# Kernel optimization log

Measured on AMD Instinct MI355X. Metric: run time of the kernel, lower is better.

Reference implementation:

```python
import jax, jax.numpy as jnp
import numpy as np

NUM_ENVS = 16384
N = 12          # decision vars (4 legs x 3D force)
M_CON = 24      # 4 SOC cones (3 each) + 12-dim hardtanh box
A_MIN, A_MAX = -10.0, 10.0
ALPHA, BETA = 1.0, 1.0


def setup_inputs() -> dict:
    key = jax.random.key(0)
    k1, k2, k3, k4 = jax.random.split(key, 4)
    Mw = jax.random.normal(k1, (NUM_ENVS, N, N), dtype=jnp.float32) / np.sqrt(N)
    # P must be SPD for inv/solve as in the original QP setup
    P = Mw @ jnp.swapaxes(Mw, -1, -2) + jnp.eye(N, dtype=jnp.float32)
    q = jax.random.normal(k2, (NUM_ENVS, N), dtype=jnp.float32)
    H = jax.random.normal(k3, (NUM_ENVS, M_CON, N), dtype=jnp.float32) * 0.5
    b = jax.random.normal(k4, (NUM_ENVS, M_CON), dtype=jnp.float32)
    contact_filter = jnp.ones((NUM_ENVS, M_CON), dtype=jnp.float32)
    return {"P": P, "q": q, "H": H, "b": b, "contact_filter": contact_filter, "iters": 100}


def _project(z, cf):
    # z: [B, m, 1]. Faithful to torch: project_onto_soc's only in-place effect on z
    # is z_part *= (z_part[:, 2:3] > 0); the full cone projection result is
    # discarded (returned but never written back). Then hardtanh box, then contact filter.
    Bsz = z.shape[0]
    soc = z[:, :12].reshape(Bsz, 4, 3)               # 4 cones of dim 3
    soc = soc * (soc[:, :, 2:3] > 0)                 # zero cone block if z-component <= 0
    box = jnp.clip(z[:, 12:24], A_MIN, A_MAX)        # hardtanh
    z = jnp.concatenate([soc.reshape(Bsz, 12, 1), box], axis=1)
    return z * cf


def reference(P, q, H, b, contact_filter, iters):
    m = H.shape[1]
    q_ = q[..., None]                                # [B, n, 1]
    b_ = b[..., None]                                # [B, m, 1]
    cf = contact_filter[..., None]                   # [B, m, 1]
    Ht = jnp.swapaxes(H, -1, -2)
    I = jnp.eye(m, dtype=P.dtype)
    Fm = I - H @ jnp.linalg.inv(P + Ht @ H) @ Ht     # [B, m, m]
    mu = Fm @ (H @ jnp.linalg.solve(P, q_) - b_)     # [B, m, 1]
    A = jnp.concatenate([
        jnp.concatenate([Fm, BETA * Fm], axis=2),
        jnp.concatenate([ALPHA * (I - 2.0 * Fm), I - 2.0 * ALPHA * BETA * Fm], axis=2),
    ], axis=1)                                       # [B, 2m, 2m]
    Bv = jnp.concatenate([BETA * mu, -2.0 * ALPHA * BETA * mu], axis=1)  # [B, 2m, 1]

    def step(lz, _):
        lz = A @ lz + Bv
        lz = jnp.concatenate([lz[:, :m], _project(lz[:, m:], cf)], axis=1)
        return lz, None

    lz0 = jnp.zeros((P.shape[0], 2 * m, 1), dtype=P.dtype)
    lz, _ = jax.lax.scan(step, lz0, None, length=iters)
    x = jnp.linalg.pinv(H) @ (lz[:, m:] - b_)        # [B, n, 1]
    return x, lz
```

## Files before the change

kernel.cpp:

```cpp
#include <hip/hip_runtime.h>

#define EPB 32
#define BLOCK 256
#define HS 292
#define GS 148
#define SS 28

#define WFENCE() __builtin_amdgcn_wave_barrier()

#define DPP_XOR1 0xB1
#define DPP_XOR2 0x4E
#define DPP_HMIR 0x141

constexpr int GMAP[8] = {0, 1, 2, 3, 7, 6, 5, 4};

typedef float f2 __attribute__((ext_vector_type(2)));

__device__ __forceinline__ f2 pkfma(f2 a, f2 b, f2 c) {
  return __builtin_elementwise_fma(a, b, c);
}

#define FMA4(acc, f, s)                                         \
  acc = fmaf((f).x, (s).x,                                      \
        fmaf((f).y, (s).y,                                      \
        fmaf((f).z, (s).z,                                      \
        fmaf((f).w, (s).w, (acc)))))

#define VFMA(acc, s, v)                                         \
  { (acc).x = fmaf((s), (v).x, (acc).x);                        \
    (acc).y = fmaf((s), (v).y, (acc).y);                        \
    (acc).z = fmaf((s), (v).z, (acc).z);                        \
    (acc).w = fmaf((s), (v).w, (acc).w); }

#define ADD4(A, B) { (A).x += (B).x; (A).y += (B).y; (A).z += (B).z; (A).w += (B).w; }

template<int CTRL>
__device__ __forceinline__ float dppv(float v) {
  return __int_as_float(__builtin_amdgcn_update_dpp(
      0, __float_as_int(v), CTRL, 0xF, 0xF, true));
}

template<int K>
__device__ __forceinline__ float getel(const float4& a, const float4& b, const float4& c) {
  if constexpr (K == 0) return a.x; else if constexpr (K == 1) return a.y;
  else if constexpr (K == 2) return a.z; else if constexpr (K == 3) return a.w;
  else if constexpr (K == 4) return b.x; else if constexpr (K == 5) return b.y;
  else if constexpr (K == 6) return b.z; else if constexpr (K == 7) return b.w;
  else if constexpr (K == 8) return c.x; else if constexpr (K == 9) return c.y;
  else if constexpr (K == 10) return c.z; else return c.w;
}
template<int K>
__device__ __forceinline__ void setel(float4& a, float4& b, float4& c, float v) {
  if constexpr (K == 0) a.x = v; else if constexpr (K == 1) a.y = v;
  else if constexpr (K == 2) a.z = v; else if constexpr (K == 3) a.w = v;
  else if constexpr (K == 4) b.x = v; else if constexpr (K == 5) b.y = v;
  else if constexpr (K == 6) b.z = v; else if constexpr (K == 7) b.w = v;
  else if constexpr (K == 8) c.x = v; else if constexpr (K == 9) c.y = v;
  else if constexpr (K == 10) c.z = v; else c.w = v;
}

template<int S>
__device__ __forceinline__ void putS2(f2* m, float v) {
  if constexpr ((S & 1) == 0) m[S / 2].x = v; else m[S / 2].y = v;
}

#define PMQ(pm, Q) make_float4(pm[2*(Q)].x, pm[2*(Q)].y, pm[2*(Q)+1].x, pm[2*(Q)+1].y)

__device__ __forceinline__ float dot12(float4 a0, float4 a1, float4 a2,
                                       const float* p) {
  const float4* p4 = (const float4*)p;
  float4 b0 = p4[0], b1 = p4[1], b2 = p4[2];
  float acc = 0.f;
  FMA4(acc, a0, b0); FMA4(acc, a1, b1); FMA4(acc, a2, b2);
  return acc;
}

template<int K>
__device__ __forceinline__ void pivot_pub(float4& a, float4& b, float4& c, float* piv) {
  float ip = 1.0f / getel<K>(a, b, c);
  setel<K>(a, b, c, 1.0f);
  a.x *= ip; a.y *= ip; a.z *= ip; a.w *= ip;
  b.x *= ip; b.y *= ip; b.z *= ip; b.w *= ip;
  c.x *= ip; c.y *= ip; c.z *= ip; c.w *= ip;
  float4* pv = (float4*)piv;
  pv[0] = a; pv[1] = b; pv[2] = c;
}

#define ELIM(f, A, B, C)                                              \
  { (A).x = fmaf(-(f), p0.x, (A).x); (A).y = fmaf(-(f), p0.y, (A).y); \
    (A).z = fmaf(-(f), p0.z, (A).z); (A).w = fmaf(-(f), p0.w, (A).w); \
    (B).x = fmaf(-(f), p1.x, (B).x); (B).y = fmaf(-(f), p1.y, (B).y); \
    (B).z = fmaf(-(f), p1.z, (B).z); (B).w = fmaf(-(f), p1.w, (B).w); \
    (C).x = fmaf(-(f), p2.x, (C).x); (C).y = fmaf(-(f), p2.y, (C).y); \
    (C).z = fmaf(-(f), p2.z, (C).z); (C).w = fmaf(-(f), p2.w, (C).w); }

template<int K>
__device__ __forceinline__ void rgj_step(float4& a0, float4& b0, float4& c0,
                                         float4& a1, float4& b1, float4& c1,
                                         float* piv, int t) {
  if constexpr (K < 8) {
    if (t == K) pivot_pub<K>(a0, b0, c0, piv);
  } else {
    if (t == K - 8) pivot_pub<K>(a1, b1, c1, piv);
  }
  WFENCE();
  const float4* pv = (const float4*)piv;
  float4 p0 = pv[0], p1 = pv[1], p2 = pv[2];
  {
    const bool own = (K < 8) && (t == K);
    float cur = getel<K>(a0, b0, c0);
    float f = own ? 0.0f : cur;
    setel<K>(a0, b0, c0, own ? cur : 0.0f);
    ELIM(f, a0, b0, c0);
  }
  {
    const bool own = (K >= 8) && (t == K - 8);
    float cur = getel<K>(a1, b1, c1);
    float f = own ? 0.0f : cur;
    setel<K>(a1, b1, c1, own ? cur : 0.0f);
    ELIM(f, a1, b1, c1);
  }
  WFENCE();
}

template<int K>
__device__ __forceinline__ void rgj_all(float4& a0, float4& b0, float4& c0,
                                        float4& a1, float4& b1, float4& c1,
                                        float* piv, int t) {
  rgj_step<K>(a0, b0, c0, a1, b1, c1, piv, t);
  if constexpr (K < 11) rgj_all<K + 1>(a0, b0, c0, a1, b1, c1, piv, t);
}

__device__ __forceinline__ void gram_rows(const float* myH, int t, int i1,
    float4& a0, float4& b0, float4& c0, float4& a1, float4& b1, float4& c1) {
  a0 = make_float4(0.f, 0.f, 0.f, 0.f);
  b0 = a0; c0 = a0; a1 = a0; b1 = a0; c1 = a0;
#pragma unroll
  for (int k = 0; k < 24; ++k) {
    const float4* hk = (const float4*)(myH + k * 12);
    float4 h0 = hk[0], h1 = hk[1], h2 = hk[2];
    float f0 = myH[k * 12 + t];
    float f1 = myH[k * 12 + i1];
    VFMA(a0, f0, h0); VFMA(b0, f0, h1); VFMA(c0, f0, h2);
    VFMA(a1, f1, h0); VFMA(b1, f1, h1); VFMA(c1, f1, h2);
  }
}

template<int g, int k>
__device__ __forceinline__ void slot3(const float* myH, int t,
    const float4* W0, const float4* W1, const float4* W2,
    f2* P0, f2* P1, f2* P2) {
  const int c = 3 * (t ^ GMAP[g]) + k;
  const float4* hc = (const float4*)(myH + c * 12);
  float4 h0 = hc[0], h1 = hc[1], h2 = hc[2];
  float d0 = 0.f, d1 = 0.f, d2 = 0.f;
  FMA4(d0, h0, W0[0]); FMA4(d0, h1, W0[1]); FMA4(d0, h2, W0[2]);
  FMA4(d1, h0, W1[0]); FMA4(d1, h1, W1[1]); FMA4(d1, h2, W1[2]);
  FMA4(d2, h0, W2[0]); FMA4(d2, h1, W2[1]); FMA4(d2, h2, W2[2]);
  constexpr int S = 3 * g + k;
  putS2<S>(P0, ((g == 0 && k == 0) ? 1.0f : 0.0f) - d0);
  putS2<S>(P1, ((g == 0 && k == 1) ? 1.0f : 0.0f) - d1);
  putS2<S>(P2, ((g == 0 && k == 2) ? 1.0f : 0.0f) - d2);
}

template<int S>
__device__ __forceinline__ float bgat(const float* bB, int t) {
  constexpr int g = S / 3, k = S % 3;
  return bB[3 * (t ^ GMAP[g]) + k];
}

__global__ __attribute__((amdgpu_flat_work_group_size(BLOCK, BLOCK),
                          amdgpu_waves_per_eu(1, 4)))
void pdhg_kernel(const float* __restrict__ P, const float* __restrict__ q,
                 const float* __restrict__ H, const float* __restrict__ b,
                 const float* __restrict__ cf, const int* __restrict__ itp,
                 float* __restrict__ out, int Btot) {
  __shared__ __align__(16) float sH[EPB * HS];
  __shared__ __align__(16) float sGi[EPB * GS];
  __shared__ __align__(16) float sB[EPB * SS];
  __shared__ __align__(16) float sAux[EPB * SS];

  const int tid  = threadIdx.x;
  const int wq   = tid >> 6;
  const int lane = tid & 63;
  const int e    = wq * 8 + (lane >> 3);
  const int t    = lane & 7;
  const int env  = blockIdx.x * EPB + e;
  const int envW0 = blockIdx.x * EPB + wq * 8;
  const int niter = itp[0];
  const int r0w = 3 * t;
  const int i1 = (t < 4) ? t + 8 : t;

  {
    const float4* gH = (const float4*)(H + (size_t)envW0 * 288);
#pragma unroll
    for (int rep = 0; rep < 9; ++rep) {
      int i = lane + rep * 64;
      int ee = i / 72, off = i - ee * 72;
      *(float4*)&sH[(wq * 8 + ee) * HS + off * 4] = gH[i];
    }
    const float4* gP = (const float4*)(P + (size_t)envW0 * 144);
#pragma unroll
    for (int rep = 0; rep < 4; ++rep) {
      int i = lane + rep * 64;
      int ee = i / 36, off = i - ee * 36;
      *(float4*)&sGi[(wq * 8 + ee) * GS + off * 4] = gP[i];
    }
    { int i = lane + 256; if (lane < 32) {
        int ee = i / 36, off = i - ee * 36;
        *(float4*)&sGi[(wq * 8 + ee) * GS + off * 4] = gP[i]; } }
    const float4* gq = (const float4*)(q + (size_t)envW0 * 12);
    if (lane < 24) {
      int ee = lane / 3, off = lane - ee * 3;
      *(float4*)&sAux[(wq * 8 + ee) * SS + off * 4] = gq[lane];
    }
    const float4* gb = (const float4*)(b + (size_t)envW0 * 24);
    if (lane < 48) {
      int ee = lane / 6, off = lane - ee * 6;
      *(float4*)&sB[(wq * 8 + ee) * SS + off * 4] = gb[lane];
    }
  }
  WFENCE();

  const float* myH = &sH[e * HS];
  float* giB  = &sGi[e * GS];
  float* auxB = &sAux[e * SS];
  float* bBm  = &sB[e * SS];
  const float* bB = bBm;

  float4 g0a, g0b, g0c, g1a, g1b, g1c;
  gram_rows(myH, t, i1, g0a, g0b, g0c, g1a, g1b, g1c);
  {
    const float4* p0 = (const float4*)(giB + t * 12);
    const float4* p1 = (const float4*)(giB + i1 * 12);
    float4 q0 = p0[0], q1 = p0[1], q2 = p0[2];
    float4 r0 = p1[0], r1 = p1[1], r2 = p1[2];
    ADD4(g0a, q0); ADD4(g0b, q1); ADD4(g0c, q2);
    ADD4(g1a, r0); ADD4(g1b, r1); ADD4(g1c, r2);
  }
  rgj_all<0>(g0a, g0b, g0c, g1a, g1b, g1c, auxB + 12, t);

  {
    float4* w0 = (float4*)(giB + t * 12);
    w0[0] = g0a; w0[1] = g0b; w0[2] = g0c;
    if (t < 4) {
      float4* w1 = (float4*)(giB + (t + 8) * 12);
      w1[0] = g1a; w1[1] = g1b; w1[2] = g1c;
    }
  }
  float y0 = dot12(g0a, g0b, g0c, auxB);
  float y1 = dot12(g1a, g1b, g1c, auxB);
  WFENCE();
  auxB[12 + t] = y0;
  if (t < 4) auxB[20 + t] = y1;
  WFENCE();

  float4 hr0[3], hr1[3], hr2[3];
  { const float4* p = (const float4*)(myH + (r0w + 0) * 12); hr0[0]=p[0]; hr0[1]=p[1]; hr0[2]=p[2]; }
  { const float4* p = (const float4*)(myH + (r0w + 1) * 12); hr1[0]=p[0]; hr1[1]=p[1]; hr1[2]=p[2]; }
  { const float4* p = (const float4*)(myH + (r0w + 2) * 12); hr2[0]=p[0]; hr2[1]=p[1]; hr2[2]=p[2]; }
  float u0, u1, u2;
  {
    const float4* y4 = (const float4*)(auxB + 12);
    float4 ya = y4[0], yb = y4[1], yc = y4[2];
    u0 = 0.f; FMA4(u0, hr0[0], ya); FMA4(u0, hr0[1], yb); FMA4(u0, hr0[2], yc);
    u1 = 0.f; FMA4(u1, hr1[0], ya); FMA4(u1, hr1[1], yb); FMA4(u1, hr1[2], yc);
    u2 = 0.f; FMA4(u2, hr2[0], ya); FMA4(u2, hr2[1], yb); FMA4(u2, hr2[2], yc);
  }

  float4 W0[3], W1[3], W2[3];
  W0[0] = make_float4(0.f,0.f,0.f,0.f); W0[1] = W0[0]; W0[2] = W0[0];
  W1[0] = W0[0]; W1[1] = W0[0]; W1[2] = W0[0];
  W2[0] = W0[0]; W2[1] = W0[0]; W2[2] = W0[0];
#define ACC_W(c, EX)                                                   \
  { const float4* g4 = (const float4*)(giB + (c) * 12);                \
    float4 r0 = g4[0], r1 = g4[1], r2 = g4[2];                         \
    float k0 = hr0[(c) >> 2].EX, k1 = hr1[(c) >> 2].EX, k2 = hr2[(c) >> 2].EX; \
    VFMA(W0[0], k0, r0); VFMA(W0[1], k0, r1); VFMA(W0[2], k0, r2);     \
    VFMA(W1[0], k1, r0); VFMA(W1[1], k1, r1); VFMA(W1[2], k1, r2);     \
    VFMA(W2[0], k2, r0); VFMA(W2[1], k2, r1); VFMA(W2[2], k2, r2); }
  ACC_W(0, x) ACC_W(1, y) ACC_W(2,  z) ACC_W(3,  w)
  ACC_W(4, x) ACC_W(5, y) ACC_W(6,  z) ACC_W(7,  w)
  ACC_W(8, x) ACC_W(9, y) ACC_W(10, z) ACC_W(11, w)
#undef ACC_W

  f2 pm0[12], pm1[12], pm2[12];
#define SL(g, k) slot3<g, k>(myH, t, W0, W1, W2, pm0, pm1, pm2);
  SL(0,0) SL(0,1) SL(0,2)  SL(1,0) SL(1,1) SL(1,2)
  SL(2,0) SL(2,1) SL(2,2)  SL(3,0) SL(3,1) SL(3,2)
  SL(4,0) SL(4,1) SL(4,2)  SL(5,0) SL(5,1) SL(5,2)
  SL(6,0) SL(6,1) SL(6,2)  SL(7,0) SL(7,1) SL(7,2)
#undef SL

  float mu0, mu1, mu2;
  {
    float4 bg0 = make_float4(bgat<0>(bB,t),  bgat<1>(bB,t),  bgat<2>(bB,t),  bgat<3>(bB,t));
    float4 bg1 = make_float4(bgat<4>(bB,t),  bgat<5>(bB,t),  bgat<6>(bB,t),  bgat<7>(bB,t));
    float4 bg2 = make_float4(bgat<8>(bB,t),  bgat<9>(bB,t),  bgat<10>(bB,t), bgat<11>(bB,t));
    float4 bg3 = make_float4(bgat<12>(bB,t), bgat<13>(bB,t), bgat<14>(bB,t), bgat<15>(bB,t));
    float4 bg4 = make_float4(bgat<16>(bB,t), bgat<17>(bB,t), bgat<18>(bB,t), bgat<19>(bB,t));
    float4 bg5 = make_float4(bgat<20>(bB,t), bgat<21>(bB,t), bgat<22>(bB,t), bgat<23>(bB,t));
    float d0 = 0.f, d1 = 0.f, d2 = 0.f;
    FMA4(d0, PMQ(pm0,0), bg0); FMA4(d1, PMQ(pm1,0), bg0); FMA4(d2, PMQ(pm2,0), bg0);
    FMA4(d0, PMQ(pm0,1), bg1); FMA4(d1, PMQ(pm1,1), bg1); FMA4(d2, PMQ(pm2,1), bg1);
    FMA4(d0, PMQ(pm0,2), bg2); FMA4(d1, PMQ(pm1,2), bg2); FMA4(d2, PMQ(pm2,2), bg2);
    FMA4(d0, PMQ(pm0,3), bg3); FMA4(d1, PMQ(pm1,3), bg3); FMA4(d2, PMQ(pm2,3), bg3);
    FMA4(d0, PMQ(pm0,4), bg4); FMA4(d1, PMQ(pm1,4), bg4); FMA4(d2, PMQ(pm2,4), bg4);
    FMA4(d0, PMQ(pm0,5), bg5); FMA4(d1, PMQ(pm1,5), bg5); FMA4(d2, PMQ(pm2,5), bg5);
    mu0 = u0 - d0;
    mu1 = u1 - d1;
    mu2 = u2 - d2;
  }
  float cfr0 = cf[(size_t)env * 24 + r0w];
  float cfr1 = cf[(size_t)env * 24 + r0w + 1];
  float cfr2 = cf[(size_t)env * 24 + r0w + 2];

  const float plo  = (t < 4) ? -3.0e38f : -10.0f;
  const float phi  = (t < 4) ?  3.0e38f :  10.0f;
  const float pthr = (t < 4) ? 0.0f     : -3.0e38f;
  float l0 = 0.f, l1 = 0.f, l2 = 0.f, z0 = 0.f, z1 = 0.f, z2 = 0.f;
#pragma unroll 2
  for (int it = 0; it < niter; ++it) {
    float s0 = l0 + z0, s1 = l1 + z1, s2 = l2 + z2;
    float g3  = dppv<DPP_XOR1>(s0), g4  = dppv<DPP_XOR1>(s1), g5  = dppv<DPP_XOR1>(s2);
    float g6  = dppv<DPP_XOR2>(s0), g7  = dppv<DPP_XOR2>(s1), g8  = dppv<DPP_XOR2>(s2);
    float g12 = dppv<DPP_HMIR>(s0), g13 = dppv<DPP_HMIR>(s1), g14 = dppv<DPP_HMIR>(s2);
    f2 vp0 = {s0, s1};
    f2 A0 = {mu0, 0.f}, A1 = {mu1, 0.f}, A2 = {mu2, 0.f};
    A0 = pkfma(pm0[0], vp0, A0); A1 = pkfma(pm1[0], vp0, A1); A2 = pkfma(pm2[0], vp0, A2);
    float g9  = dppv<DPP_XOR2>(g3),  g10 = dppv<DPP_XOR2>(g4),  g11 = dppv<DPP_XOR2>(g5);
    float g15 = dppv<DPP_HMIR>(g3),  g16 = dppv<DPP_HMIR>(g4),  g17 = dppv<DPP_HMIR>(g5);
    float g18 = dppv<DPP_HMIR>(g6),  g19 = dppv<DPP_HMIR>(g7),  g20 = dppv<DPP_HMIR>(g8);
    f2 vp1 = {s2, g3}, vp2 = {g4, g5}, vp3 = {g6, g7};
    A0 = pkfma(pm0[1], vp1, A0); A1 = pkfma(pm1[1], vp1, A1); A2 = pkfma(pm2[1], vp1, A2);
    A0 = pkfma(pm0[2], vp2, A0); A1 = pkfma(pm1[2], vp2, A1); A2 = pkfma(pm2[2], vp2, A2);
    A0 = pkfma(pm0[3], vp3, A0); A1 = pkfma(pm1[3], vp3, A1); A2 = pkfma(pm2[3], vp3, A2);
    float g21 = dppv<DPP_HMIR>(g9), g22 = dppv<DPP_HMIR>(g10), g23 = dppv<DPP_HMIR>(g11);
    f2 vp4 = {g8, g9}, vp5 = {g10, g11};
    A0 = pkfma(pm0[4], vp4, A0); A1 = pkfma(pm1[4], vp4, A1); A2 = pkfma(pm2[4], vp4, A2);
    A0 = pkfma(pm0[5], vp5, A0); A1 = pkfma(pm1[5], vp5, A1); A2 = pkfma(pm2[5], vp5, A2);
    f2 vp6 = {g12, g13}, vp7 = {g14, g15}, vp8 = {g16, g17}, vp9 = {g18, g19};
    f2 B0 = {0.f, 0.f}, B1 = {0.f, 0.f}, B2 = {0.f, 0.f};
    B0 = pkfma(pm0[6], vp6, B0); B1 = pkfma(pm1[6], vp6, B1); B2 = pkfma(pm2[6], vp6, B2);
    B0 = pkfma(pm0[7], vp7, B0); B1 = pkfma(pm1[7], vp7, B1); B2 = pkfma(pm2[7], vp7, B2);
    B0 = pkfma(pm0[8], vp8, B0); B1 = pkfma(pm1[8], vp8, B1); B2 = pkfma(pm2[8], vp8, B2);
    B0 = pkfma(pm0[9], vp9, B0); B1 = pkfma(pm1[9], vp9, B1); B2 = pkfma(pm2[9], vp9, B2);
    f2 vp10 = {g20, g21}, vp11 = {g22, g23};
    B0 = pkfma(pm0[10], vp10, B0); B1 = pkfma(pm1[10], vp10, B1); B2 = pkfma(pm2[10], vp10, B2);
    B0 = pkfma(pm0[11], vp11, B0); B1 = pkfma(pm1[11], vp11, B1); B2 = pkfma(pm2[11], vp11, B2);
    f2 C0 = A0 + B0, C1 = A1 + B1, C2 = A2 + B2;
    float w0 = C0.x + C0.y, w1 = C1.x + C1.y, w2 = C2.x + C2.y;
    float zp0 = fmaf(-2.0f, w0, s0);
    float zp1 = fmaf(-2.0f, w1, s1);
    float zp2 = fmaf(-2.0f, w2, s2);
    l0 = w0; l1 = w1; l2 = w2;
    bool gt = zp2 > pthr;
    float e0 = gt ? cfr0 : 0.0f;
    float e1 = gt ? cfr1 : 0.0f;
    float e2 = gt ? cfr2 : 0.0f;
    z0 = __builtin_amdgcn_fmed3f(zp0, plo, phi) * e0;
    z1 = __builtin_amdgcn_fmed3f(zp1, plo, phi) * e1;
    z2 = __builtin_amdgcn_fmed3f(zp2, plo, phi) * e2;
  }

  float* xout  = out;
  float* lzout = out + (size_t)Btot * 12;
  lzout[(size_t)env * 48 + r0w]          = l0;
  lzout[(size_t)env * 48 + r0w + 1]      = l1;
  lzout[(size_t)env * 48 + r0w + 2]      = l2;
  lzout[(size_t)env * 48 + 24 + r0w]     = z0;
  lzout[(size_t)env * 48 + 24 + r0w + 1] = z1;
  lzout[(size_t)env * 48 + 24 + r0w + 2] = z2;

  float bo0 = bB[r0w];
  float bo1 = bB[r0w + 1];
  float bo2 = bB[r0w + 2];
  WFENCE();
  auxB[r0w]     = z0 - bo0;
  auxB[r0w + 1] = z1 - bo1;
  auxB[r0w + 2] = z2 - bo2;
  WFENCE();

  float rv0 = 0.f, rv8 = 0.f;
  {
    const float4* a4 = (const float4*)auxB;
    float4 au0 = a4[0], au1 = a4[1], au2 = a4[2], au3 = a4[3], au4 = a4[4], au5 = a4[5];
#define RVS(k, AV) { rv0 = fmaf(myH[(k) * 12 + t],  (AV), rv0);   \
                     rv8 = fmaf(myH[(k) * 12 + i1], (AV), rv8); }
    RVS(0,  au0.x) RVS(1,  au0.y) RVS(2,  au0.z) RVS(3,  au0.w)
    RVS(4,  au1.x) RVS(5,  au1.y) RVS(6,  au1.z) RVS(7,  au1.w)
    RVS(8,  au2.x) RVS(9,  au2.y) RVS(10, au2.z) RVS(11, au2.w)
    RVS(12, au3.x) RVS(13, au3.y) RVS(14, au3.z) RVS(15, au3.w)
    RVS(16, au4.x) RVS(17, au4.y) RVS(18, au4.z) RVS(19, au4.w)
    RVS(20, au5.x) RVS(21, au5.y) RVS(22, au5.z) RVS(23, au5.w)
#undef RVS
  }

  gram_rows(myH, t, i1, g0a, g0b, g0c, g1a, g1b, g1c);
  WFENCE();
  auxB[t] = rv0;
  if (t < 4) auxB[t + 8] = rv8;
  WFENCE();
  rgj_all<0>(g0a, g0b, g0c, g1a, g1b, g1c, bBm, t);

  xout[(size_t)env * 12 + t] = dot12(g0a, g0b, g0c, auxB);
  if (t < 4)
    xout[(size_t)env * 12 + t + 8] = dot12(g1a, g1b, g1c, auxB);
}

extern "C" void kernel_launch(void* const* d_in, const int* in_sizes, int n_in,
                              void* d_out, int out_size, void* d_ws, size_t ws_size,
                              hipStream_t stream) {
  const float* P  = (const float*)d_in[0];
  const float* q  = (const float*)d_in[1];
  const float* H  = (const float*)d_in[2];
  const float* b  = (const float*)d_in[3];
  const float* cf = (const float*)d_in[4];
  const int*   it = (const int*)d_in[5];
  float* out = (float*)d_out;
  const int B = in_sizes[1] / 12;
  const int grid = B / EPB;
  pdhg_kernel<<<grid, BLOCK, 0, stream>>>(P, q, H, b, cf, it, out, B);
}
```

Before: 139.6 us.

## Remap to four lanes per env with six rows each, halving block size

Each environment is now handled by 4 lanes instead of 8. Each lane owns 6 rows of the 24-row iteration matrix, using 72 packed coefficients instead of 36. The 128-thread block still covers 32 envs, so each wave processes 16 envs. The change drops the 8-lane DPP mirror gather in favour of quad-level XOR and quad-permute shuffles, and the Gauss-Jordan solve now spreads 3 rows per lane. This cuts cross-lane shuffles per useful FMA and removes the lane imbalance in the 12-row solves, at the cost of doubling register pressure for the coefficient arrays, which could lower occupancy or cause spills.

```diff
diff --git a/kernel.cpp b/kernel.cpp
--- a/kernel.cpp
+++ b/kernel.cpp
@@ -1,7 +1,7 @@
 #include <hip/hip_runtime.h>
 
 #define EPB 32
-#define BLOCK 256
+#define BLOCK 128
 #define HS 292
 #define GS 148
 #define SS 28
@@ -10,9 +10,7 @@
 
 #define DPP_XOR1 0xB1
 #define DPP_XOR2 0x4E
-#define DPP_HMIR 0x141
-
-constexpr int GMAP[8] = {0, 1, 2, 3, 7, 6, 5, 4};
+#define DPP_QP3  0x1B
 
 typedef float f2 __attribute__((ext_vector_type(2)));
 
@@ -58,13 +56,6 @@
   else if constexpr (K == 8) c.x = v; else if constexpr (K == 9) c.y = v;
   else if constexpr (K == 10) c.z = v; else c.w = v;
 }
-
-template<int S>
-__device__ __forceinline__ void putS2(f2* m, float v) {
-  if constexpr ((S & 1) == 0) m[S / 2].x = v; else m[S / 2].y = v;
-}
-
-#define PMQ(pm, Q) make_float4(pm[2*(Q)].x, pm[2*(Q)].y, pm[2*(Q)+1].x, pm[2*(Q)+1].y)
 
 __device__ __forceinline__ float dot12(float4 a0, float4 a1, float4 a2,
                                        const float* p) {
@@ -95,79 +86,135 @@
     (C).z = fmaf(-(f), p2.z, (C).z); (C).w = fmaf(-(f), p2.w, (C).w); }
 
 template<int K>
-__device__ __forceinline__ void rgj_step(float4& a0, float4& b0, float4& c0,
-                                         float4& a1, float4& b1, float4& c1,
-                                         float* piv, int t) {
-  if constexpr (K < 8) {
-    if (t == K) pivot_pub<K>(a0, b0, c0, piv);
-  } else {
-    if (t == K - 8) pivot_pub<K>(a1, b1, c1, piv);
+__device__ __forceinline__ void rgj3_step(
+    float4& a0, float4& b0, float4& c0,
+    float4& a1, float4& b1, float4& c1,
+    float4& a2, float4& b2, float4& c2,
+    float* piv, int t) {
+  constexpr int SET = K >> 2, OWN = K & 3;
+  if (t == OWN) {
+    if constexpr (SET == 0)      pivot_pub<K>(a0, b0, c0, piv);
+    else if constexpr (SET == 1) pivot_pub<K>(a1, b1, c1, piv);
+    else                         pivot_pub<K>(a2, b2, c2, piv);
   }
   WFENCE();
   const float4* pv = (const float4*)piv;
   float4 p0 = pv[0], p1 = pv[1], p2 = pv[2];
   {
-    const bool own = (K < 8) && (t == K);
+    const bool own = (SET == 0) && (t == OWN);
     float cur = getel<K>(a0, b0, c0);
     float f = own ? 0.0f : cur;
     setel<K>(a0, b0, c0, own ? cur : 0.0f);
     ELIM(f, a0, b0, c0);
   }
   {
-    const bool own = (K >= 8) && (t == K - 8);
+    const bool own = (SET == 1) && (t == OWN);
     float cur = getel<K>(a1, b1, c1);
     float f = own ? 0.0f : cur;
     setel<K>(a1, b1, c1, own ? cur : 0.0f);
     ELIM(f, a1, b1, c1);
   }
+  {
+    const bool own = (SET == 2) && (t == OWN);
+    float cur = getel<K>(a2, b2, c2);
+    float f = own ? 0.0f : cur;
+    setel<K>(a2, b2, c2, own ? cur : 0.0f);
+    ELIM(f, a2, b2, c2);
+  }
   WFENCE();
 }
 
 template<int K>
-__device__ __forceinline__ void rgj_all(float4& a0, float4& b0, float4& c0,
-                                        float4& a1, float4& b1, float4& c1,
-                                        float* piv, int t) {
-  rgj_step<K>(a0, b0, c0, a1, b1, c1, piv, t);
-  if constexpr (K < 11) rgj_all<K + 1>(a0, b0, c0, a1, b1, c1, piv, t);
-}
-
-__device__ __forceinline__ void gram_rows(const float* myH, int t, int i1,
-    float4& a0, float4& b0, float4& c0, float4& a1, float4& b1, float4& c1) {
+__device__ __forceinline__ void rgj3_all(
+    float4& a0, float4& b0, float4& c0,
+    float4& a1, float4& b1, float4& c1,
+    float4& a2, float4& b2, float4& c2,
+    float* piv, int t) {
+  rgj3_step<K>(a0, b0, c0, a1, b1, c1, a2, b2, c2, piv, t);
+  if constexpr (K < 11) rgj3_all<K + 1>(a0, b0, c0, a1, b1, c1, a2, b2, c2, piv, t);
+}
+
+__device__ __forceinline__ void gram3(const float* myH, int t,
+    float4& a0, float4& b0, float4& c0,
+    float4& a1, float4& b1, float4& c1,
+    float4& a2, float4& b2, float4& c2) {
   a0 = make_float4(0.f, 0.f, 0.f, 0.f);
-  b0 = a0; c0 = a0; a1 = a0; b1 = a0; c1 = a0;
+  b0 = a0; c0 = a0; a1 = a0; b1 = a0; c1 = a0; a2 = a0; b2 = a0; c2 = a0;
 #pragma unroll
   for (int k = 0; k < 24; ++k) {
     const float4* hk = (const float4*)(myH + k * 12);
     float4 h0 = hk[0], h1 = hk[1], h2 = hk[2];
     float f0 = myH[k * 12 + t];
-    float f1 = myH[k * 12 + i1];
-    VFMA(a0, f0, h0); VFMA(b0, f0, h1); VFMA(c0, f0, h2);
-    VFMA(a1, f1, h0); VFMA(b1, f1, h1); VFMA(c1, f1, h2);
-  }
-}
-
-template<int g, int k>
-__device__ __forceinline__ void slot3(const float* myH, int t,
-    const float4* W0, const float4* W1, const float4* W2,
-    f2* P0, f2* P1, f2* P2) {
-  const int c = 3 * (t ^ GMAP[g]) + k;
+    float f1 = myH[k * 12 + t + 4];
+    float f2v = myH[k * 12 + t + 8];
+    VFMA(a0, f0, h0);  VFMA(b0, f0, h1);  VFMA(c0, f0, h2);
+    VFMA(a1, f1, h0);  VFMA(b1, f1, h1);  VFMA(c1, f1, h2);
+    VFMA(a2, f2v, h0); VFMA(b2, f2v, h1); VFMA(c2, f2v, h2);
+  }
+}
+
+__device__ __forceinline__ void buildW(const float* myH, const float* gi, int r0,
+                                       float4* Wa, float4* Wb, float4* Wc) {
+  Wa[0] = make_float4(0.f, 0.f, 0.f, 0.f); Wa[1] = Wa[0]; Wa[2] = Wa[0];
+  Wb[0] = Wa[0]; Wb[1] = Wa[0]; Wb[2] = Wa[0];
+  Wc[0] = Wa[0]; Wc[1] = Wa[0]; Wc[2] = Wa[0];
+#pragma unroll
+  for (int c = 0; c < 12; ++c) {
+    const float4* g4 = (const float4*)(gi + c * 12);
+    float4 r0v = g4[0], r1v = g4[1], r2v = g4[2];
+    float k0 = myH[(r0 + 0) * 12 + c];
+    float k1 = myH[(r0 + 1) * 12 + c];
+    float k2 = myH[(r0 + 2) * 12 + c];
+    VFMA(Wa[0], k0, r0v); VFMA(Wa[1], k0, r1v); VFMA(Wa[2], k0, r2v);
+    VFMA(Wb[0], k1, r0v); VFMA(Wb[1], k1, r1v); VFMA(Wb[2], k1, r2v);
+    VFMA(Wc[0], k2, r0v); VFMA(Wc[1], k2, r1v); VFMA(Wc[2], k2, r2v);
+  }
+}
+
+template<int m, int k, int base>
+__device__ __forceinline__ void slot4(const float* myH, int t,
+    const float4* Wa, const float4* Wb, const float4* Wc,
+    f2* pA, f2* pB, f2* pC) {
+  const int c = 6 * (t ^ m) + k;
   const float4* hc = (const float4*)(myH + c * 12);
   float4 h0 = hc[0], h1 = hc[1], h2 = hc[2];
   float d0 = 0.f, d1 = 0.f, d2 = 0.f;
-  FMA4(d0, h0, W0[0]); FMA4(d0, h1, W0[1]); FMA4(d0, h2, W0[2]);
-  FMA4(d1, h0, W1[0]); FMA4(d1, h1, W1[1]); FMA4(d1, h2, W1[2]);
-  FMA4(d2, h0, W2[0]); FMA4(d2, h1, W2[1]); FMA4(d2, h2, W2[2]);
-  constexpr int S = 3 * g + k;
-  putS2<S>(P0, ((g == 0 && k == 0) ? 1.0f : 0.0f) - d0);
-  putS2<S>(P1, ((g == 0 && k == 1) ? 1.0f : 0.0f) - d1);
-  putS2<S>(P2, ((g == 0 && k == 2) ? 1.0f : 0.0f) - d2);
-}
-
-template<int S>
-__device__ __forceinline__ float bgat(const float* bB, int t) {
-  constexpr int g = S / 3, k = S % 3;
-  return bB[3 * (t ^ GMAP[g]) + k];
-}
+  FMA4(d0, h0, Wa[0]); FMA4(d0, h1, Wa[1]); FMA4(d0, h2, Wa[2]);
+  FMA4(d1, h0, Wb[0]); FMA4(d1, h1, Wb[1]); FMA4(d1, h2, Wb[2]);
+  FMA4(d2, h0, Wc[0]); FMA4(d2, h1, Wc[1]); FMA4(d2, h2, Wc[2]);
+  float v0 = ((m == 0 && k == base + 0) ? 1.0f : 0.0f) - d0;
+  float v1 = ((m == 0 && k == base + 1) ? 1.0f : 0.0f) - d1;
+  float v2 = ((m == 0 && k == base + 2) ? 1.0f : 0.0f) - d2;
+  constexpr int P = 3 * m + (k >> 1);
+  if constexpr ((k & 1) == 0) { pA[P].x = v0; pB[P].x = v1; pC[P].x = v2; }
+  else                        { pA[P].y = v0; pB[P].y = v1; pC[P].y = v2; }
+}
+
+#define SLOTS(base, pA, pB, pC)                                   \
+  slot4<0,0,base>(myH,t,Wa,Wb,Wc,pA,pB,pC);                       \
+  slot4<0,1,base>(myH,t,Wa,Wb,Wc,pA,pB,pC);                       \
+  slot4<0,2,base>(myH,t,Wa,Wb,Wc,pA,pB,pC);                       \
+  slot4<0,3,base>(myH,t,Wa,Wb,Wc,pA,pB,pC);                       \
+  slot4<0,4,base>(myH,t,Wa,Wb,Wc,pA,pB,pC);                       \
+  slot4<0,5,base>(myH,t,Wa,Wb,Wc,pA,pB,pC);                       \
+  slot4<1,0,base>(myH,t,Wa,Wb,Wc,pA,pB,pC);                       \
+  slot4<1,1,base>(myH,t,Wa,Wb,Wc,pA,pB,pC);                       \
+  slot4<1,2,base>(myH,t,Wa,Wb,Wc,pA,pB,pC);                       \
+  slot4<1,3,base>(myH,t,Wa,Wb,Wc,pA,pB,pC);                       \
+  slot4<1,4,base>(myH,t,Wa,Wb,Wc,pA,pB,pC);                       \
+  slot4<1,5,base>(myH,t,Wa,Wb,Wc,pA,pB,pC);                       \
+  slot4<2,0,base>(myH,t,Wa,Wb,Wc,pA,pB,pC);                       \
+  slot4<2,1,base>(myH,t,Wa,Wb,Wc,pA,pB,pC);                       \
+  slot4<2,2,base>(myH,t,Wa,Wb,Wc,pA,pB,pC);                       \
+  slot4<2,3,base>(myH,t,Wa,Wb,Wc,pA,pB,pC);                       \
+  slot4<2,4,base>(myH,t,Wa,Wb,Wc,pA,pB,pC);                       \
+  slot4<2,5,base>(myH,t,Wa,Wb,Wc,pA,pB,pC);                       \
+  slot4<3,0,base>(myH,t,Wa,Wb,Wc,pA,pB,pC);                       \
+  slot4<3,1,base>(myH,t,Wa,Wb,Wc,pA,pB,pC);                       \
+  slot4<3,2,base>(myH,t,Wa,Wb,Wc,pA,pB,pC);                       \
+  slot4<3,3,base>(myH,t,Wa,Wb,Wc,pA,pB,pC);                       \
+  slot4<3,4,base>(myH,t,Wa,Wb,Wc,pA,pB,pC);                       \
+  slot4<3,5,base>(myH,t,Wa,Wb,Wc,pA,pB,pC);
 
 __global__ __attribute__((amdgpu_flat_work_group_size(BLOCK, BLOCK),
                           amdgpu_waves_per_eu(1, 4)))
@@ -183,41 +230,44 @@
   const int tid  = threadIdx.x;
   const int wq   = tid >> 6;
   const int lane = tid & 63;
-  const int e    = wq * 8 + (lane >> 3);
-  const int t    = lane & 7;
+  const int g16  = lane >> 2;
+  const int t    = lane & 3;
+  const int e    = wq * 16 + g16;
   const int env  = blockIdx.x * EPB + e;
-  const int envW0 = blockIdx.x * EPB + wq * 8;
+  const int envW0 = blockIdx.x * EPB + wq * 16;
   const int niter = itp[0];
-  const int r0w = 3 * t;
-  const int i1 = (t < 4) ? t + 8 : t;
+  const int r6 = 6 * t;
 
   {
     const float4* gH = (const float4*)(H + (size_t)envW0 * 288);
+#pragma unroll
+    for (int rep = 0; rep < 18; ++rep) {
+      int i = lane + rep * 64;
+      int ee = i / 72, off = i - ee * 72;
+      *(float4*)&sH[(wq * 16 + ee) * HS + off * 4] = gH[i];
+    }
+    const float4* gP = (const float4*)(P + (size_t)envW0 * 144);
 #pragma unroll
     for (int rep = 0; rep < 9; ++rep) {
       int i = lane + rep * 64;
-      int ee = i / 72, off = i - ee * 72;
-      *(float4*)&sH[(wq * 8 + ee) * HS + off * 4] = gH[i];
+      int ee = i / 36, off = i - ee * 36;
+      *(float4*)&sGi[(wq * 16 + ee) * GS + off * 4] = gP[i];
     }
-    const float4* gP = (const float4*)(P + (size_t)envW0 * 144);
-#pragma unroll
-    for (int rep = 0; rep < 4; ++rep) {
-      int i = lane + rep * 64;
-      int ee = i / 36, off = i - ee * 36;
-      *(float4*)&sGi[(wq * 8 + ee) * GS + off * 4] = gP[i];
-    }
-    { int i = lane + 256; if (lane < 32) {
-        int ee = i / 36, off = i - ee * 36;
-        *(float4*)&sGi[(wq * 8 + ee) * GS + off * 4] = gP[i]; } }
     const float4* gq = (const float4*)(q + (size_t)envW0 * 12);
-    if (lane < 24) {
+    if (lane < 48) {
       int ee = lane / 3, off = lane - ee * 3;
-      *(float4*)&sAux[(wq * 8 + ee) * SS + off * 4] = gq[lane];
+      *(float4*)&sAux[(wq * 16 + ee) * SS + off * 4] = gq[lane];
     }
     const float4* gb = (const float4*)(b + (size_t)envW0 * 24);
-    if (lane < 48) {
-      int ee = lane / 6, off = lane - ee * 6;
-      *(float4*)&sB[(wq * 8 + ee) * SS + off * 4] = gb[lane];
+    {
+      int i = lane;
+      int ee = i / 6, off = i - ee * 6;
+      *(float4*)&sB[(wq * 16 + ee) * SS + off * 4] = gb[i];
+      if (lane < 32) {
+        i = lane + 64;
+        ee = i / 6; off = i - ee * 6;
+        *(float4*)&sB[(wq * 16 + ee) * SS + off * 4] = gb[i];
+      }
     }
   }
   WFENCE();
@@ -228,165 +278,181 @@
   float* bBm  = &sB[e * SS];
   const float* bB = bBm;
 
-  float4 g0a, g0b, g0c, g1a, g1b, g1c;
-  gram_rows(myH, t, i1, g0a, g0b, g0c, g1a, g1b, g1c);
+  float4 a0, b0, c0, a1, b1, c1, a2, b2, c2;
+  gram3(myH, t, a0, b0, c0, a1, b1, c1, a2, b2, c2);
   {
     const float4* p0 = (const float4*)(giB + t * 12);
-    const float4* p1 = (const float4*)(giB + i1 * 12);
+    const float4* p1 = (const float4*)(giB + (t + 4) * 12);
+    const float4* p2 = (const float4*)(giB + (t + 8) * 12);
     float4 q0 = p0[0], q1 = p0[1], q2 = p0[2];
     float4 r0 = p1[0], r1 = p1[1], r2 = p1[2];
-    ADD4(g0a, q0); ADD4(g0b, q1); ADD4(g0c, q2);
-    ADD4(g1a, r0); ADD4(g1b, r1); ADD4(g1c, r2);
-  }
-  rgj_all<0>(g0a, g0b, g0c, g1a, g1b, g1c, auxB + 12, t);
-
-  {
-    float4* w0 = (float4*)(giB + t * 12);
-    w0[0] = g0a; w0[1] = g0b; w0[2] = g0c;
-    if (t < 4) {
-      float4* w1 = (float4*)(giB + (t + 8) * 12);
-      w1[0] = g1a; w1[1] = g1b; w1[2] = g1c;
-    }
-  }
-  float y0 = dot12(g0a, g0b, g0c, auxB);
-  float y1 = dot12(g1a, g1b, g1c, auxB);
-  WFENCE();
-  auxB[12 + t] = y0;
-  if (t < 4) auxB[20 + t] = y1;
-  WFENCE();
-
-  float4 hr0[3], hr1[3], hr2[3];
-  { const float4* p = (const float4*)(myH + (r0w + 0) * 12); hr0[0]=p[0]; hr0[1]=p[1]; hr0[2]=p[2]; }
-  { const float4* p = (const float4*)(myH + (r0w + 1) * 12); hr1[0]=p[0]; hr1[1]=p[1]; hr1[2]=p[2]; }
-  { const float4* p = (const float4*)(myH + (r0w + 2) * 12); hr2[0]=p[0]; hr2[1]=p[1]; hr2[2]=p[2]; }
-  float u0, u1, u2;
+    float4 s0 = p2[0], s1 = p2[1], s2 = p2[2];
+    ADD4(a0, q0); ADD4(b0, q1); ADD4(c0, q2);
+    ADD4(a1, r0); ADD4(b1, r1); ADD4(c1, r2);
+    ADD4(a2, s0); ADD4(b2, s1); ADD4(c2, s2);
+  }
+  rgj3_all<0>(a0, b0, c0, a1, b1, c1, a2, b2, c2, auxB + 12, t);
+
+  {
+    float4* w0 = (float4*)(giB + t * 12);        w0[0] = a0; w0[1] = b0; w0[2] = c0;
+    float4* w1 = (float4*)(giB + (t + 4) * 12);  w1[0] = a1; w1[1] = b1; w1[2] = c1;
+    float4* w2 = (float4*)(giB + (t + 8) * 12);  w2[0] = a2; w2[1] = b2; w2[2] = c2;
+  }
+  float y0 = dot12(a0, b0, c0, auxB);
+  float y1 = dot12(a1, b1, c1, auxB);
+  float y2 = dot12(a2, b2, c2, auxB);
+  WFENCE();
+  auxB[12 + t] = y0; auxB[16 + t] = y1; auxB[20 + t] = y2;
+  WFENCE();
+
+  float u0, u1, u2, u3, u4, u5;
   {
     const float4* y4 = (const float4*)(auxB + 12);
     float4 ya = y4[0], yb = y4[1], yc = y4[2];
-    u0 = 0.f; FMA4(u0, hr0[0], ya); FMA4(u0, hr0[1], yb); FMA4(u0, hr0[2], yc);
-    u1 = 0.f; FMA4(u1, hr1[0], ya); FMA4(u1, hr1[1], yb); FMA4(u1, hr1[2], yc);
-    u2 = 0.f; FMA4(u2, hr2[0], ya); FMA4(u2, hr2[1], yb); FMA4(u2, hr2[2], yc);
-  }
-
-  float4 W0[3], W1[3], W2[3];
-  W0[0] = make_float4(0.f,0.f,0.f,0.f); W0[1] = W0[0]; W0[2] = W0[0];
-  W1[0] = W0[0]; W1[1] = W0[0]; W1[2] = W0[0];
-  W2[0] = W0[0]; W2[1] = W0[0]; W2[2] = W0[0];
-#define ACC_W(c, EX)                                                   \
-  { const float4* g4 = (const float4*)(giB + (c) * 12);                \
-    float4 r0 = g4[0], r1 = g4[1], r2 = g4[2];                         \
-    float k0 = hr0[(c) >> 2].EX, k1 = hr1[(c) >> 2].EX, k2 = hr2[(c) >> 2].EX; \
-    VFMA(W0[0], k0, r0); VFMA(W0[1], k0, r1); VFMA(W0[2], k0, r2);     \
-    VFMA(W1[0], k1, r0); VFMA(W1[1], k1, r1); VFMA(W1[2], k1, r2);     \
-    VFMA(W2[0], k2, r0); VFMA(W2[1], k2, r1); VFMA(W2[2], k2, r2); }
-  ACC_W(0, x) ACC_W(1, y) ACC_W(2,  z) ACC_W(3,  w)
-  ACC_W(4, x) ACC_W(5, y) ACC_W(6,  z) ACC_W(7,  w)
-  ACC_W(8, x) ACC_W(9, y) ACC_W(10, z) ACC_W(11, w)
-#undef ACC_W
-
-  f2 pm0[12], pm1[12], pm2[12];
-#define SL(g, k) slot3<g, k>(myH, t, W0, W1, W2, pm0, pm1, pm2);
-  SL(0,0) SL(0,1) SL(0,2)  SL(1,0) SL(1,1) SL(1,2)
-  SL(2,0) SL(2,1) SL(2,2)  SL(3,0) SL(3,1) SL(3,2)
-  SL(4,0) SL(4,1) SL(4,2)  SL(5,0) SL(5,1) SL(5,2)
-  SL(6,0) SL(6,1) SL(6,2)  SL(7,0) SL(7,1) SL(7,2)
-#undef SL
-
-  float mu0, mu1, mu2;
-  {
-    float4 bg0 = make_float4(bgat<0>(bB,t),  bgat<1>(bB,t),  bgat<2>(bB,t),  bgat<3>(bB,t));
-    float4 bg1 = make_float4(bgat<4>(bB,t),  bgat<5>(bB,t),  bgat<6>(bB,t),  bgat<7>(bB,t));
-    float4 bg2 = make_float4(bgat<8>(bB,t),  bgat<9>(bB,t),  bgat<10>(bB,t), bgat<11>(bB,t));
-    float4 bg3 = make_float4(bgat<12>(bB,t), bgat<13>(bB,t), bgat<14>(bB,t), bgat<15>(bB,t));
-    float4 bg4 = make_float4(bgat<16>(bB,t), bgat<17>(bB,t), bgat<18>(bB,t), bgat<19>(bB,t));
-    float4 bg5 = make_float4(bgat<20>(bB,t), bgat<21>(bB,t), bgat<22>(bB,t), bgat<23>(bB,t));
-    float d0 = 0.f, d1 = 0.f, d2 = 0.f;
-    FMA4(d0, PMQ(pm0,0), bg0); FMA4(d1, PMQ(pm1,0), bg0); FMA4(d2, PMQ(pm2,0), bg0);
-    FMA4(d0, PMQ(pm0,1), bg1); FMA4(d1, PMQ(pm1,1), bg1); FMA4(d2, PMQ(pm2,1), bg1);
-    FMA4(d0, PMQ(pm0,2), bg2); FMA4(d1, PMQ(pm1,2), bg2); FMA4(d2, PMQ(pm2,2), bg2);
-    FMA4(d0, PMQ(pm0,3), bg3); FMA4(d1, PMQ(pm1,3), bg3); FMA4(d2, PMQ(pm2,3), bg3);
-    FMA4(d0, PMQ(pm0,4), bg4); FMA4(d1, PMQ(pm1,4), bg4); FMA4(d2, PMQ(pm2,4), bg4);
-    FMA4(d0, PMQ(pm0,5), bg5); FMA4(d1, PMQ(pm1,5), bg5); FMA4(d2, PMQ(pm2,5), bg5);
-    mu0 = u0 - d0;
-    mu1 = u1 - d1;
-    mu2 = u2 - d2;
-  }
-  float cfr0 = cf[(size_t)env * 24 + r0w];
-  float cfr1 = cf[(size_t)env * 24 + r0w + 1];
-  float cfr2 = cf[(size_t)env * 24 + r0w + 2];
-
-  const float plo  = (t < 4) ? -3.0e38f : -10.0f;
-  const float phi  = (t < 4) ?  3.0e38f :  10.0f;
-  const float pthr = (t < 4) ? 0.0f     : -3.0e38f;
-  float l0 = 0.f, l1 = 0.f, l2 = 0.f, z0 = 0.f, z1 = 0.f, z2 = 0.f;
+#define UROW(rr, dst) { const float4* hp = (const float4*)(myH + (r6 + (rr)) * 12); \
+      float4 h0 = hp[0], h1 = hp[1], h2 = hp[2]; dst = 0.f;                         \
+      FMA4(dst, h0, ya); FMA4(dst, h1, yb); FMA4(dst, h2, yc); }
+    UROW(0, u0) UROW(1, u1) UROW(2, u2) UROW(3, u3) UROW(4, u4) UROW(5, u5)
+#undef UROW
+  }
+
+  f2 pm0_[12], pm1_[12], pm2_[12], pm3_[12], pm4_[12], pm5_[12];
+  {
+    float4 Wa[3], Wb[3], Wc[3];
+    buildW(myH, giB, r6 + 0, Wa, Wb, Wc);
+    SLOTS(0, pm0_, pm1_, pm2_)
+    buildW(myH, giB, r6 + 3, Wa, Wb, Wc);
+    SLOTS(3, pm3_, pm4_, pm5_)
+  }
+
+  float mu0, mu1, mu2, mu3, mu4, mu5;
+  {
+    const int cA = 6 * (t ^ 1), cB = 6 * (t ^ 2), cC = 6 * (t ^ 3);
+    f2 bq0 = { bB[r6 + 0], bB[r6 + 1] };
+    f2 bq1 = { bB[r6 + 2], bB[r6 + 3] };
+    f2 bq2 = { bB[r6 + 4], bB[r6 + 5] };
+    f2 bq3 = { bB[cA + 0], bB[cA + 1] };
+    f2 bq4 = { bB[cA + 2], bB[cA + 3] };
+    f2 bq5 = { bB[cA + 4], bB[cA + 5] };
+    f2 bq6 = { bB[cB + 0], bB[cB + 1] };
+    f2 bq7 = { bB[cB + 2], bB[cB + 3] };
+    f2 bq8 = { bB[cB + 4], bB[cB + 5] };
+    f2 bq9 = { bB[cC + 0], bB[cC + 1] };
+    f2 bq10 = { bB[cC + 2], bB[cC + 3] };
+    f2 bq11 = { bB[cC + 4], bB[cC + 5] };
+#define MUROW(rr, uu) {                                              \
+    f2 S1 = {0.f, 0.f}, S2 = {0.f, 0.f};                             \
+    S1 = pkfma(pm##rr##_[0], bq0, S1);                               \
+    S1 = pkfma(pm##rr##_[1], bq1, S1);                               \
+    S1 = pkfma(pm##rr##_[2], bq2, S1);                               \
+    S1 = pkfma(pm##rr##_[3], bq3, S1);                               \
+    S1 = pkfma(pm##rr##_[4], bq4, S1);                               \
+    S1 = pkfma(pm##rr##_[5], bq5, S1);                               \
+    S2 = pkfma(pm##rr##_[6], bq6, S2);                               \
+    S2 = pkfma(pm##rr##_[7], bq7, S2);                               \
+    S2 = pkfma(pm##rr##_[8], bq8, S2);                               \
+    S2 = pkfma(pm##rr##_[9], bq9, S2);                               \
+    S2 = pkfma(pm##rr##_[10], bq10, S2);                             \
+    S2 = pkfma(pm##rr##_[11], bq11, S2);                             \
+    f2 St = S1 + S2;                                                 \
+    mu##rr = (uu) - (St.x + St.y); }
+    MUROW(0, u0) MUROW(1, u1) MUROW(2, u2)
+    MUROW(3, u3) MUROW(4, u4) MUROW(5, u5)
+#undef MUROW
+  }
+  const float* cfp = cf + (size_t)env * 24 + r6;
+  float cfv0 = cfp[0], cfv1 = cfp[1], cfv2 = cfp[2];
+  float cfv3 = cfp[3], cfv4 = cfp[4], cfv5 = cfp[5];
+
+  const float plo  = (t < 2) ? -3.0e38f : -10.0f;
+  const float phi  = (t < 2) ?  3.0e38f :  10.0f;
+  const float pthr = (t < 2) ? 0.0f     : -3.0e38f;
+  float l0 = 0.f, l1 = 0.f, l2 = 0.f, l3 = 0.f, l4 = 0.f, l5 = 0.f;
+  float z0 = 0.f, z1 = 0.f, z2 = 0.f, z3 = 0.f, z4 = 0.f, z5 = 0.f;
 #pragma unroll 2
   for (int it = 0; it < niter; ++it) {
-    float s0 = l0 + z0, s1 = l1 + z1, s2 = l2 + z2;
-    float g3  = dppv<DPP_XOR1>(s0), g4  = dppv<DPP_XOR1>(s1), g5  = dppv<DPP_XOR1>(s2);
-    float g6  = dppv<DPP_XOR2>(s0), g7  = dppv<DPP_XOR2>(s1), g8  = dppv<DPP_XOR2>(s2);
-    float g12 = dppv<DPP_HMIR>(s0), g13 = dppv<DPP_HMIR>(s1), g14 = dppv<DPP_HMIR>(s2);
-    f2 vp0 = {s0, s1};
-    f2 A0 = {mu0, 0.f}, A1 = {mu1, 0.f}, A2 = {mu2, 0.f};
-    A0 = pkfma(pm0[0], vp0, A0); A1 = pkfma(pm1[0], vp0, A1); A2 = pkfma(pm2[0], vp0, A2);
-    float g9  = dppv<DPP_XOR2>(g3),  g10 = dppv<DPP_XOR2>(g4),  g11 = dppv<DPP_XOR2>(g5);
-    float g15 = dppv<DPP_HMIR>(g3),  g16 = dppv<DPP_HMIR>(g4),  g17 = dppv<DPP_HMIR>(g5);
-    float g18 = dppv<DPP_HMIR>(g6),  g19 = dppv<DPP_HMIR>(g7),  g20 = dppv<DPP_HMIR>(g8);
-    f2 vp1 = {s2, g3}, vp2 = {g4, g5}, vp3 = {g6, g7};
-    A0 = pkfma(pm0[1], vp1, A0); A1 = pkfma(pm1[1], vp1, A1); A2 = pkfma(pm2[1], vp1, A2);
-    A0 = pkfma(pm0[2], vp2, A0); A1 = pkfma(pm1[2], vp2, A1); A2 = pkfma(pm2[2], vp2, A2);
-    A0 = pkfma(pm0[3], vp3, A0); A1 = pkfma(pm1[3], vp3, A1); A2 = pkfma(pm2[3], vp3, A2);
-    float g21 = dppv<DPP_HMIR>(g9), g22 = dppv<DPP_HMIR>(g10), g23 = dppv<DPP_HMIR>(g11);
-    f2 vp4 = {g8, g9}, vp5 = {g10, g11};
-    A0 = pkfma(pm0[4], vp4, A0); A1 = pkfma(pm1[4], vp4, A1); A2 = pkfma(pm2[4], vp4, A2);
-    A0 = pkfma(pm0[5], vp5, A0); A1 = pkfma(pm1[5], vp5, A1); A2 = pkfma(pm2[5], vp5, A2);
-    f2 vp6 = {g12, g13}, vp7 = {g14, g15}, vp8 = {g16, g17}, vp9 = {g18, g19};
-    f2 B0 = {0.f, 0.f}, B1 = {0.f, 0.f}, B2 = {0.f, 0.f};
-    B0 = pkfma(pm0[6], vp6, B0); B1 = pkfma(pm1[6], vp6, B1); B2 = pkfma(pm2[6], vp6, B2);
-    B0 = pkfma(pm0[7], vp7, B0); B1 = pkfma(pm1[7], vp7, B1); B2 = pkfma(pm2[7], vp7, B2);
-    B0 = pkfma(pm0[8], vp8, B0); B1 = pkfma(pm1[8], vp8, B1); B2 = pkfma(pm2[8], vp8, B2);
-    B0 = pkfma(pm0[9], vp9, B0); B1 = pkfma(pm1[9], vp9, B1); B2 = pkfma(pm2[9], vp9, B2);
-    f2 vp10 = {g20, g21}, vp11 = {g22, g23};
-    B0 = pkfma(pm0[10], vp10, B0); B1 = pkfma(pm1[10], vp10, B1); B2 = pkfma(pm2[10], vp10, B2);
-    B0 = pkfma(pm0[11], vp11, B0); B1 = pkfma(pm1[11], vp11, B1); B2 = pkfma(pm2[11], vp11, B2);
-    f2 C0 = A0 + B0, C1 = A1 + B1, C2 = A2 + B2;
-    float w0 = C0.x + C0.y, w1 = C1.x + C1.y, w2 = C2.x + C2.y;
-    float zp0 = fmaf(-2.0f, w0, s0);
-    float zp1 = fmaf(-2.0f, w1, s1);
-    float zp2 = fmaf(-2.0f, w2, s2);
-    l0 = w0; l1 = w1; l2 = w2;
-    bool gt = zp2 > pthr;
-    float e0 = gt ? cfr0 : 0.0f;
-    float e1 = gt ? cfr1 : 0.0f;
-    float e2 = gt ? cfr2 : 0.0f;
+    f2 q0, q1, q2;
+    q0.x = l0 + z0; q0.y = l1 + z1;
+    q1.x = l2 + z2; q1.y = l3 + z3;
+    q2.x = l4 + z4; q2.y = l5 + z5;
+    f2 q3, q4, q5, q6, q7, q8, q9, q10, q11;
+    q3.x = dppv<DPP_XOR1>(q0.x);  q3.y = dppv<DPP_XOR1>(q0.y);
+    q4.x = dppv<DPP_XOR1>(q1.x);  q4.y = dppv<DPP_XOR1>(q1.y);
+    q5.x = dppv<DPP_XOR1>(q2.x);  q5.y = dppv<DPP_XOR1>(q2.y);
+    q6.x = dppv<DPP_XOR2>(q0.x);  q6.y = dppv<DPP_XOR2>(q0.y);
+    q7.x = dppv<DPP_XOR2>(q1.x);  q7.y = dppv<DPP_XOR2>(q1.y);
+    q8.x = dppv<DPP_XOR2>(q2.x);  q8.y = dppv<DPP_XOR2>(q2.y);
+    q9.x = dppv<DPP_QP3>(q0.x);   q9.y = dppv<DPP_QP3>(q0.y);
+    q10.x = dppv<DPP_QP3>(q1.x);  q10.y = dppv<DPP_QP3>(q1.y);
+    q11.x = dppv<DPP_QP3>(q2.x);  q11.y = dppv<DPP_QP3>(q2.y);
+#define FMAROW(rr, wdst) {                                           \
+    f2 A = { mu##rr, 0.f };                                          \
+    f2 Bv = { 0.f, 0.f };                                            \
+    A = pkfma(pm##rr##_[0], q0, A);                                  \
+    A = pkfma(pm##rr##_[1], q1, A);                                  \
+    A = pkfma(pm##rr##_[2], q2, A);                                  \
+    A = pkfma(pm##rr##_[3], q3, A);                                  \
+    A = pkfma(pm##rr##_[4], q4, A);                                  \
+    A = pkfma(pm##rr##_[5], q5, A);                                  \
+    Bv = pkfma(pm##rr##_[6], q6, Bv);                                \
+    Bv = pkfma(pm##rr##_[7], q7, Bv);                                \
+    Bv = pkfma(pm##rr##_[8], q8, Bv);                                \
+    Bv = pkfma(pm##rr##_[9], q9, Bv);                                \
+    Bv = pkfma(pm##rr##_[10], q10, Bv);                              \
+    Bv = pkfma(pm##rr##_[11], q11, Bv);                              \
+    f2 C = A + Bv;                                                   \
+    wdst = C.x + C.y; }
+    float w0, w1, w2, w3, w4, w5;
+    FMAROW(0, w0) FMAROW(1, w1) FMAROW(2, w2)
+    FMAROW(3, w3) FMAROW(4, w4) FMAROW(5, w5)
+#undef FMAROW
+    float zp0 = fmaf(-2.0f, w0, q0.x);
+    float zp1 = fmaf(-2.0f, w1, q0.y);
+    float zp2 = fmaf(-2.0f, w2, q1.x);
+    float zp3 = fmaf(-2.0f, w3, q1.y);
+    float zp4 = fmaf(-2.0f, w4, q2.x);
+    float zp5 = fmaf(-2.0f, w5, q2.y);
+    l0 = w0; l1 = w1; l2 = w2; l3 = w3; l4 = w4; l5 = w5;
+    bool gA = zp2 > pthr;
+    bool gB = zp5 > pthr;
+    float e0 = gA ? cfv0 : 0.0f;
+    float e1 = gA ? cfv1 : 0.0f;
+    float e2 = gA ? cfv2 : 0.0f;
+    float e3 = gB ? cfv3 : 0.0f;
+    float e4 = gB ? cfv4 : 0.0f;
+    float e5 = gB ? cfv5 : 0.0f;
     z0 = __builtin_amdgcn_fmed3f(zp0, plo, phi) * e0;
     z1 = __builtin_amdgcn_fmed3f(zp1, plo, phi) * e1;
     z2 = __builtin_amdgcn_fmed3f(zp2, plo, phi) * e2;
+    z3 = __builtin_amdgcn_fmed3f(zp3, plo, phi) * e3;
+    z4 = __builtin_amdgcn_fmed3f(zp4, plo, phi) * e4;
+    z5 = __builtin_amdgcn_fmed3f(zp5, plo, phi) * e5;
   }
 
   float* xout  = out;
   float* lzout = out + (size_t)Btot * 12;
-  lzout[(size_t)env * 48 + r0w]          = l0;
-  lzout[(size_t)env * 48 + r0w + 1]      = l1;
-  lzout[(size_t)env * 48 + r0w + 2]      = l2;
-  lzout[(size_t)env * 48 + 24 + r0w]     = z0;
-  lzout[(size_t)env * 48 + 24 + r0w + 1] = z1;
-  lzout[(size_t)env * 48 + 24 + r0w + 2] = z2;
-
-  float bo0 = bB[r0w];
-  float bo1 = bB[r0w + 1];
-  float bo2 = bB[r0w + 2];
-  WFENCE();
-  auxB[r0w]     = z0 - bo0;
-  auxB[r0w + 1] = z1 - bo1;
-  auxB[r0w + 2] = z2 - bo2;
-  WFENCE();
-
-  float rv0 = 0.f, rv8 = 0.f;
+  {
+    size_t base = (size_t)env * 48 + r6;
+    lzout[base + 0] = l0; lzout[base + 1] = l1; lzout[base + 2] = l2;
+    lzout[base + 3] = l3; lzout[base + 4] = l4; lzout[base + 5] = l5;
+    lzout[base + 24 + 0] = z0; lzout[base + 24 + 1] = z1; lzout[base + 24 + 2] = z2;
+    lzout[base + 24 + 3] = z3; lzout[base + 24 + 4] = z4; lzout[base + 24 + 5] = z5;
+  }
+
+  float bo0 = bB[r6 + 0], bo1 = bB[r6 + 1], bo2 = bB[r6 + 2];
+  float bo3 = bB[r6 + 3], bo4 = bB[r6 + 4], bo5 = bB[r6 + 5];
+  WFENCE();
+  auxB[r6 + 0] = z0 - bo0; auxB[r6 + 1] = z1 - bo1; auxB[r6 + 2] = z2 - bo2;
+  auxB[r6 + 3] = z3 - bo3; auxB[r6 + 4] = z4 - bo4; auxB[r6 + 5] = z5 - bo5;
+  WFENCE();
+
+  float rv0 = 0.f, rv1 = 0.f, rv2 = 0.f;
   {
     const float4* a4 = (const float4*)auxB;
     float4 au0 = a4[0], au1 = a4[1], au2 = a4[2], au3 = a4[3], au4 = a4[4], au5 = a4[5];
-#define RVS(k, AV) { rv0 = fmaf(myH[(k) * 12 + t],  (AV), rv0);   \
-                     rv8 = fmaf(myH[(k) * 12 + i1], (AV), rv8); }
+#define RVS(k, AV) { rv0 = fmaf(myH[(k) * 12 + t],     (AV), rv0);  \
+                     rv1 = fmaf(myH[(k) * 12 + t + 4], (AV), rv1);  \
+                     rv2 = fmaf(myH[(k) * 12 + t + 8], (AV), rv2); }
     RVS(0,  au0.x) RVS(1,  au0.y) RVS(2,  au0.z) RVS(3,  au0.w)
     RVS(4,  au1.x) RVS(5,  au1.y) RVS(6,  au1.z) RVS(7,  au1.w)
     RVS(8,  au2.x) RVS(9,  au2.y) RVS(10, au2.z) RVS(11, au2.w)
@@ -396,16 +462,15 @@
 #undef RVS
   }
 
-  gram_rows(myH, t, i1, g0a, g0b, g0c, g1a, g1b, g1c);
-  WFENCE();
-  auxB[t] = rv0;
-  if (t < 4) auxB[t + 8] = rv8;
-  WFENCE();
-  rgj_all<0>(g0a, g0b, g0c, g1a, g1b, g1c, bBm, t);
-
-  xout[(size_t)env * 12 + t] = dot12(g0a, g0b, g0c, auxB);
-  if (t < 4)
-    xout[(size_t)env * 12 + t + 8] = dot12(g1a, g1b, g1c, auxB);
+  gram3(myH, t, a0, b0, c0, a1, b1, c1, a2, b2, c2);
+  WFENCE();
+  auxB[t] = rv0; auxB[t + 4] = rv1; auxB[t + 8] = rv2;
+  WFENCE();
+  rgj3_all<0>(a0, b0, c0, a1, b1, c1, a2, b2, c2, bBm, t);
+
+  xout[(size_t)env * 12 + t]     = dot12(a0, b0, c0, auxB);
+  xout[(size_t)env * 12 + t + 4] = dot12(a1, b1, c1, auxB);
+  xout[(size_t)env * 12 + t + 8] = dot12(a2, b2, c2, auxB);
 }
 
 extern "C" void kernel_launch(void* const* d_in, const int* in_sizes, int n_in,
```

Measured after the change: 132.1 us. 1.06x faster.
